# Kernel tuning notes

Hardware: AMD Instinct MI355X
Metric: run time of the kernel (lower is better)

## Reference

```python
import jax, jax.numpy as jnp
import numpy as np

D_MODEL = 1024
NUM_HEADS = 16
HEAD_DIM = D_MODEL // NUM_HEADS


def setup_inputs() -> dict:
    key = jax.random.key(0)
    ks = jax.random.split(key, 9)
    B, S = 2, 2048
    s = 1.0 / np.sqrt(D_MODEL)
    inp = {
        "x": jax.random.normal(ks[0], (B, S, D_MODEL), dtype=jnp.float32),
        "Wq": jax.random.normal(ks[1], (D_MODEL, D_MODEL), dtype=jnp.float32) * s,
        "bq": jnp.zeros((D_MODEL,), dtype=jnp.float32),
        "Wk": jax.random.normal(ks[2], (D_MODEL, D_MODEL), dtype=jnp.float32) * s,
        "bk": jnp.zeros((D_MODEL,), dtype=jnp.float32),
        "Wv": jax.random.normal(ks[3], (D_MODEL, D_MODEL), dtype=jnp.float32) * s,
        "bv": jnp.zeros((D_MODEL,), dtype=jnp.float32),
        "Wo": jax.random.normal(ks[4], (D_MODEL, D_MODEL), dtype=jnp.float32) * s,
        "bo": jnpp if False else jnp.zeros((D_MODEL,), dtype=jnp.float32),
    }
    return inp


def reference(x, Wq, bq, Wk, bk, Wv, bv, Wo, bo):
    B, S, D = x.shape
    H, hd = NUM_HEADS, HEAD_DIM
    # QKV projections (Linear: x @ W^T + b), split into heads -> [B,H,S,hd]
    q = (x @ Wq.T + bq).reshape(B, S, H, hd).transpose(0, 2, 1, 3)
    k = (x @ Wk.T + bk).reshape(B, S, H, hd).transpose(0, 2, 1, 3)
    v = (x @ Wv.T + bv).reshape(B, S, H, hd).transpose(0, 2, 1, 3)
    # scores [B,H,S,S]
    scores = jnp.einsum('bhqd,bhkd->bhqk', q, k) / jnp.sqrt(jnp.float32(hd))
    p = jax.nn.softmax(scores, axis=-1)
    out = jnp.einsum('bhqk,bhkd->bhqd', p, v)  # [B,H,S,hd]
    out = out.transpose(0, 2, 1, 3).reshape(B, S, D)
    return out @ Wo.T + bo
```

## Files before the change

kernel.cpp:

```cpp
#include <hip/hip_runtime.h>
#include <hip/hip_bf16.h>
#include <math.h>

typedef __bf16 bf16;
typedef unsigned short u16;
typedef __bf16 bf16x8 __attribute__((ext_vector_type(8)));
typedef __bf16 bf16x4 __attribute__((ext_vector_type(4)));
typedef short  s16x4  __attribute__((ext_vector_type(4)));
typedef float  f32x4  __attribute__((ext_vector_type(4)));

#define D_MODEL 1024
#define NHEAD   16
#define HD      64
#define BATCH   2
#define SEQ     2048
#define MTOT    (BATCH*SEQ)

#define EXPSCALE 0.18033688011116016f

__device__ __forceinline__ void async16(const void* g, void* l) {
    __builtin_amdgcn_global_load_lds(
        (__attribute__((address_space(1))) unsigned int*)g,
        (__attribute__((address_space(3))) unsigned int*)l,
        16, 0, 0);
}

__device__ __forceinline__ f32x4 mfma16(s16x4 a, s16x4 b, f32x4 c) {
    return __builtin_amdgcn_mfma_f32_16x16x16bf16_1k(a, b, c, 0, 0, 0);
}

__global__ __launch_bounds__(256) void cast_kernel(
    const float* __restrict__ x,
    const float* __restrict__ wq, const float* __restrict__ wk,
    const float* __restrict__ wv, const float* __restrict__ wo,
    bf16* __restrict__ xb, bf16* __restrict__ wqb, bf16* __restrict__ wkb,
    bf16* __restrict__ wvb, bf16* __restrict__ wob)
{
    const int z = blockIdx.y;
    const float* src;
    bf16* dst;
    int n;
    if (z == 0)      { src = x;  dst = xb;  n = MTOT * D_MODEL; }
    else if (z == 1) { src = wq; dst = wqb; n = D_MODEL * D_MODEL; }
    else if (z == 2) { src = wk; dst = wkb; n = D_MODEL * D_MODEL; }
    else if (z == 3) { src = wv; dst = wvb; n = D_MODEL * D_MODEL; }
    else             { src = wo; dst = wob; n = D_MODEL * D_MODEL; }

    int i = (blockIdx.x * 256 + threadIdx.x) * 8;
    if (i >= n) return;
    float4 a = *(const float4*)(src + i);
    float4 b = *(const float4*)(src + i + 4);
    bf16x8 o;
    o[0] = (bf16)a.x; o[1] = (bf16)a.y; o[2] = (bf16)a.z; o[3] = (bf16)a.w;
    o[4] = (bf16)b.x; o[5] = (bf16)b.y; o[6] = (bf16)b.z; o[7] = (bf16)b.w;
    *(bf16x8*)(dst + i) = o;
}

__device__ __forceinline__ void gemm_core(const bf16* __restrict__ A,
                                          const bf16* __restrict__ W,
                                          int m0, int n0,
                                          f32x4 acc[4][4],
                                          u16* lA, u16* lB)
{
    const int tid  = threadIdx.x;
    const int lane = tid & 63;
    const int wave = tid >> 6;
    const int wr   = wave >> 1;
    const int wc   = wave & 1;
    const int fr   = lane & 15;
    const int quad = lane >> 4;

    #pragma unroll
    for (int mi = 0; mi < 4; ++mi)
        #pragma unroll
        for (int ni = 0; ni < 4; ++ni)
            #pragma unroll
            for (int e = 0; e < 4; ++e)
                acc[mi][ni][e] = 0.0f;

    const int row = tid >> 3;
    const int ca  = ((tid & 7) ^ (row & 7)) * 8;
    const bf16* gA[4];
    const bf16* gB[4];
    u16 *sA[4], *sB[4];
    #pragma unroll
    for (int c = 0; c < 4; ++c) {
        int slot = tid + c * 256;
        int r    = row + c * 32;
        gA[c] = A + (size_t)(m0 + r) * 1024 + ca;
        gB[c] = W + (size_t)(n0 + r) * 1024 + ca;
        sA[c] = lA + (size_t)slot * 8;
        sB[c] = lB + (size_t)slot * 8;
    }

    for (int kt = 0; kt < 1024 / 64; ++kt) {
        __syncthreads();
        #pragma unroll
        for (int c = 0; c < 4; ++c) {
            async16(gA[c] + kt * 64, sA[c]);
            async16(gB[c] + kt * 64, sB[c]);
        }
        __syncthreads();

        #pragma unroll
        for (int ks = 0; ks < 2; ++ks) {
            const int sa = ((ks * 4 + quad) ^ (fr & 7)) * 8;
            bf16x8 af[4], bfm[4];
            #pragma unroll
            for (int mi = 0; mi < 4; ++mi)
                af[mi] = *(const bf16x8*)(lA + (wr * 64 + mi * 16 + fr) * 64 + sa);
            #pragma unroll
            for (int ni = 0; ni < 4; ++ni)
                bfm[ni] = *(const bf16x8*)(lB + (wc * 64 + ni * 16 + fr) * 64 + sa);

            #pragma unroll
            for (int mi = 0; mi < 4; ++mi)
                #pragma unroll
                for (int ni = 0; ni < 4; ++ni)
                    acc[mi][ni] = __builtin_amdgcn_mfma_f32_16x16x32_bf16(
                        af[mi], bfm[ni], acc[mi][ni], 0, 0, 0);
        }
    }
}

__global__ __launch_bounds__(256) void qkv_kernel(
    const bf16* __restrict__ x,
    const bf16* __restrict__ Wq, const bf16* __restrict__ Wk, const bf16* __restrict__ Wv,
    const float* __restrict__ bq, const float* __restrict__ bk, const float* __restrict__ bv,
    bf16* __restrict__ Q, bf16* __restrict__ K, bf16* __restrict__ Vt)
{
    __shared__ __align__(16) u16 lA[128 * 64];
    __shared__ __align__(16) u16 lB[128 * 64];

    const int z = blockIdx.z;
    int m0, n0;
    const bf16 *mA, *mB;
    const float* bias;
    if (z == 2) {
        mA = Wv; mB = x; bias = bv;
        m0 = blockIdx.y * 128;
        n0 = blockIdx.x * 128;
    } else {
        mA = x;  mB = (z == 0) ? Wq : Wk; bias = (z == 0) ? bq : bk;
        m0 = blockIdx.x * 128;
        n0 = blockIdx.y * 128;
    }

    f32x4 acc[4][4];
    gemm_core(mA, mB, m0, n0, acc, lA, lB);

    const int lane = threadIdx.x & 63;
    const int wave = threadIdx.x >> 6;
    const int wr = wave >> 1, wc = wave & 1;
    const int col = lane & 15, quad = lane >> 4;

    if (z == 2) {
        #pragma unroll
        for (int mi = 0; mi < 4; ++mi) {
            #pragma unroll
            for (int ni = 0; ni < 4; ++ni) {
                #pragma unroll
                for (int r = 0; r < 4; ++r) {
                    int f = m0 + wr * 64 + mi * 16 + quad * 4 + r;
                    int t = n0 + wc * 64 + ni * 16 + col;
                    float v = acc[mi][ni][r] + bias[f];
                    int b = t >> 11, s = t & 2047;
                    int h = f >> 6,  d = f & 63;
                    Vt[((size_t)(b * NHEAD + h) * HD + d) * SEQ + s] = (bf16)v;
                }
            }
        }
    } else {
        const float qs = (z == 0) ? EXPSCALE : 1.0f;
        bf16* o = (z == 0) ? Q : K;
        #pragma unroll
        for (int mi = 0; mi < 4; ++mi) {
            #pragma unroll
            for (int ni = 0; ni < 4; ++ni) {
                #pragma unroll
                for (int r = 0; r < 4; ++r) {
                    int m = m0 + wr * 64 + mi * 16 + quad * 4 + r;
                    int n = n0 + wc * 64 + ni * 16 + col;
                    float v = (acc[mi][ni][r] + bias[n]) * qs;
                    int b = m >> 11, s = m & 2047;
                    int h = n >> 6,  d = n & 63;
                    o[((size_t)(b * NHEAD + h) * SEQ + s) * HD + d] = (bf16)v;
                }
            }
        }
    }
}

__global__ __launch_bounds__(256, 2) void attn_kernel(
    const bf16* __restrict__ Q, const bf16* __restrict__ K,
    const bf16* __restrict__ Vt, bf16* __restrict__ O)
{
    __shared__ __align__(16) u16 lK[2][64 * 64];
    __shared__ __align__(16) u16 lV[2][64 * 64];

    const int tid  = threadIdx.x;
    const int lane = tid & 63;
    const int wave = tid >> 6;
    const int col  = lane & 15;
    const int quad = lane >> 4;
    const int bh   = blockIdx.x;
    const int q0   = blockIdx.y * 128;

    const bf16* Qh = Q  + (size_t)bh * SEQ * HD;
    const bf16* Kh = K  + (size_t)bh * SEQ * HD;
    const bf16* Vh = Vt + (size_t)bh * HD * SEQ;

    bf16x8 qf[2][2];
    #pragma unroll
    for (int qb = 0; qb < 2; ++qb)
        #pragma unroll
        for (int ks = 0; ks < 2; ++ks)
            qf[qb][ks] = *(const bf16x8*)(
                Qh + (size_t)(q0 + wave * 32 + qb * 16 + col) * HD + ks * 32 + quad * 8);

    f32x4 acc_o[2][4];
    #pragma unroll
    for (int qb = 0; qb < 2; ++qb)
        #pragma unroll
        for (int nd = 0; nd < 4; ++nd)
            #pragma unroll
            for (int e = 0; e < 4; ++e) acc_o[qb][nd][e] = 0.0f;
    float rs[2] = {0.0f, 0.0f};
    const f32x4 zero4 = {0.0f, 0.0f, 0.0f, 0.0f};

    const int r0 = tid >> 3;
    const int r1 = r0 + 32;
    const int g0 = (((tid & 7) ^ (r0 & 7))) * 8;
    const int g1 = (((tid & 7) ^ (r1 & 7))) * 8;
    const bf16* gK0 = Kh + (size_t)r0 * HD + g0;
    const bf16* gK1 = Kh + (size_t)r1 * HD + g1;
    const bf16* gV0 = Vh + (size_t)r0 * SEQ + g0;
    const bf16* gV1 = Vh + (size_t)r1 * SEQ + g1;
    const int so0 = tid * 8;
    const int so1 = (tid + 256) * 8;

    async16(gK0, lK[0] + so0);
    async16(gK1, lK[0] + so1);
    async16(gV0, lV[0] + so0);
    async16(gV1, lV[0] + so1);

    int cur = 0;
    for (int jt = 0; jt < SEQ / 64; ++jt) {
        __syncthreads();

        if (jt + 1 < SEQ / 64) {
            const int nx = cur ^ 1;
            async16(gK0 + (size_t)(jt + 1) * 64 * HD, lK[nx] + so0);
            async16(gK1 + (size_t)(jt + 1) * 64 * HD, lK[nx] + so1);
            async16(gV0 + (jt + 1) * 64, lV[nx] + so0);
            async16(gV1 + (jt + 1) * 64, lV[nx] + so1);
        }

        const u16* K_ = lK[cur];
        const u16* V_ = lV[cur];

        f32x4 sc[2][4];
        #pragma unroll
        for (int nj = 0; nj < 4; ++nj) {
            bf16x8 kf0 = *(const bf16x8*)(
                K_ + (nj * 16 + col) * 64 + ((0 + quad) ^ (col & 7)) * 8);
            sc[0][nj] = __builtin_amdgcn_mfma_f32_16x16x32_bf16(kf0, qf[0][0], zero4, 0, 0, 0);
            sc[1][nj] = __builtin_amdgcn_mfma_f32_16x16x32_bf16(kf0, qf[1][0], zero4, 0, 0, 0);
        }
        #pragma unroll
        for (int nj = 0; nj < 4; ++nj) {
            bf16x8 kf1 = *(const bf16x8*)(
                K_ + (nj * 16 + col) * 64 + ((4 + quad) ^ (col & 7)) * 8);
            sc[0][nj] = __builtin_amdgcn_mfma_f32_16x16x32_bf16(kf1, qf[0][1], sc[0][nj], 0, 0, 0);
            sc[1][nj] = __builtin_amdgcn_mfma_f32_16x16x32_bf16(kf1, qf[1][1], sc[1][nj], 0, 0, 0);
        }

        s16x4 pb[2][4];
        #pragma unroll
        for (int qb = 0; qb < 2; ++qb) {
            #pragma unroll
            for (int nj = 0; nj < 4; ++nj) {
                float p0 = __builtin_amdgcn_exp2f(sc[qb][nj][0]);
                float p1 = __builtin_amdgcn_exp2f(sc[qb][nj][1]);
                float p2 = __builtin_amdgcn_exp2f(sc[qb][nj][2]);
                float p3 = __builtin_amdgcn_exp2f(sc[qb][nj][3]);
                rs[qb] += (p0 + p1) + (p2 + p3);
                bf16x4 t;
                t[0] = (bf16)p0; t[1] = (bf16)p1; t[2] = (bf16)p2; t[3] = (bf16)p3;
                pb[qb][nj] = __builtin_bit_cast(s16x4, t);
            }
        }

        #pragma unroll
        for (int nj = 0; nj < 4; ++nj) {
            #pragma unroll
            for (int nd = 0; nd < 4; ++nd) {
                int row = nd * 16 + col;
                int jb  = (2 * nj + (quad >> 1)) ^ (row & 7);
                s16x4 vb = *(const s16x4*)(V_ + row * 64 + jb * 8 + (quad & 1) * 4);
                acc_o[0][nd] = mfma16(pb[0][nj], vb, acc_o[0][nd]);
                acc_o[1][nd] = mfma16(pb[1][nj], vb, acc_o[1][nd]);
            }
        }

        cur ^= 1;
    }

    const int b = bh >> 4, h = bh & 15;
    #pragma unroll
    for (int qb = 0; qb < 2; ++qb) {
        float v = rs[qb];
        v += __shfl_xor(v, 16);
        v += __shfl_xor(v, 32);
        float inv = 1.0f / v;
        float invr[4];
        #pragma unroll
        for (int r = 0; r < 4; ++r)
            invr[r] = __shfl(inv, quad * 4 + r);
        #pragma unroll
        for (int nd = 0; nd < 4; ++nd) {
            #pragma unroll
            for (int r = 0; r < 4; ++r) {
                int srow = q0 + wave * 32 + qb * 16 + quad * 4 + r;
                int d    = nd * 16 + col;
                float o  = acc_o[qb][nd][r] * invr[r];
                O[((size_t)(b * SEQ + srow)) * D_MODEL + h * HD + d] = (bf16)o;
            }
        }
    }
}

__global__ __launch_bounds__(256) void oproj_kernel(
    const bf16* __restrict__ A, const bf16* __restrict__ Wo,
    const float* __restrict__ bo, float* __restrict__ out)
{
    __shared__ __align__(16) u16 lA[128 * 64];
    __shared__ __align__(16) u16 lB[64 * 64];

    const int m0 = blockIdx.x * 128;
    const int n0 = blockIdx.y * 64;

    const int tid  = threadIdx.x;
    const int lane = tid & 63;
    const int wave = tid >> 6;
    const int wr   = wave >> 1;
    const int wc   = wave & 1;
    const int fr   = lane & 15;
    const int quad = lane >> 4;

    f32x4 acc[4][2];
    #pragma unroll
    for (int mi = 0; mi < 4; ++mi)
        #pragma unroll
        for (int ni = 0; ni < 2; ++ni)
            #pragma unroll
            for (int e = 0; e < 4; ++e)
                acc[mi][ni][e] = 0.0f;

    const int row = tid >> 3;
    const int ca  = ((tid & 7) ^ (row & 7)) * 8;
    const bf16* gA[4];
    u16* sA[4];
    #pragma unroll
    for (int c = 0; c < 4; ++c) {
        int slot = tid + c * 256;
        gA[c] = A + (size_t)(m0 + row + c * 32) * 1024 + ca;
        sA[c] = lA + (size_t)slot * 8;
    }
    const bf16* gB[2];
    u16* sB[2];
    #pragma unroll
    for (int c = 0; c < 2; ++c) {
        int slot = tid + c * 256;
        gB[c] = Wo + (size_t)(n0 + row + c * 32) * 1024 + ca;
        sB[c] = lB + (size_t)slot * 8;
    }

    for (int kt = 0; kt < 1024 / 64; ++kt) {
        __syncthreads();
        #pragma unroll
        for (int c = 0; c < 4; ++c) async16(gA[c] + kt * 64, sA[c]);
        #pragma unroll
        for (int c = 0; c < 2; ++c) async16(gB[c] + kt * 64, sB[c]);
        __syncthreads();

        #pragma unroll
        for (int ks = 0; ks < 2; ++ks) {
            const int sa = ((ks * 4 + quad) ^ (fr & 7)) * 8;
            bf16x8 af[4], bfm[2];
            #pragma unroll
            for (int mi = 0; mi < 4; ++mi)
                af[mi] = *(const bf16x8*)(lA + (wr * 64 + mi * 16 + fr) * 64 + sa);
            #pragma unroll
            for (int ni = 0; ni < 2; ++ni)
                bfm[ni] = *(const bf16x8*)(lB + (wc * 32 + ni * 16 + fr) * 64 + sa);

            #pragma unroll
            for (int mi = 0; mi < 4; ++mi)
                #pragma unroll
                for (int ni = 0; ni < 2; ++ni)
                    acc[mi][ni] = __builtin_amdgcn_mfma_f32_16x16x32_bf16(
                        af[mi], bfm[ni], acc[mi][ni], 0, 0, 0);
        }
    }

    const int col = fr;
    #pragma unroll
    for (int mi = 0; mi < 4; ++mi) {
        #pragma unroll
        for (int ni = 0; ni < 2; ++ni) {
            #pragma unroll
            for (int r = 0; r < 4; ++r) {
                int m = m0 + wr * 64 + mi * 16 + quad * 4 + r;
                int n = n0 + wc * 32 + ni * 16 + col;
                out[(size_t)m * D_MODEL + n] = acc[mi][ni][r] + bo[n];
            }
        }
    }
}

extern "C" void kernel_launch(void* const* d_in, const int* in_sizes, int n_in,
                              void* d_out, int out_size, void* d_ws, size_t ws_size,
                              hipStream_t stream)
{
    const float* x  = (const float*)d_in[0];
    const float* Wq = (const float*)d_in[1];
    const float* bq = (const float*)d_in[2];
    const float* Wk = (const float*)d_in[3];
    const float* bk = (const float*)d_in[4];
    const float* Wv = (const float*)d_in[5];
    const float* bv = (const float*)d_in[6];
    const float* Wo = (const float*)d_in[7];
    const float* bo = (const float*)d_in[8];
    float* out = (float*)d_out;

    char* ws = (char*)d_ws;
    const size_t XSZ = (size_t)MTOT * D_MODEL * sizeof(bf16);
    const size_t WSZ = (size_t)D_MODEL * D_MODEL * sizeof(bf16);
    bf16* wqb = (bf16*)(ws);
    bf16* wkb = (bf16*)(ws + WSZ);
    bf16* wvb = (bf16*)(ws + 2 * WSZ);
    bf16* wob = (bf16*)(ws + 3 * WSZ);
    bf16* xb  = (bf16*)(ws + 4 * WSZ);
    bf16* Qb  = (bf16*)(ws + 4 * WSZ + XSZ);
    bf16* Kb  = (bf16*)(ws + 4 * WSZ + 2 * XSZ);
    bf16* Vt  = (bf16*)(ws + 4 * WSZ + 3 * XSZ);
    bf16* At  = (bf16*)(ws + 4 * WSZ + 4 * XSZ);

    cast_kernel<<<dim3((MTOT * D_MODEL) / (256 * 8), 5), 256, 0, stream>>>(
        x, Wq, Wk, Wv, Wo, xb, wqb, wkb, wvb, wob);

    qkv_kernel<<<dim3(32, 8, 3), 256, 0, stream>>>(
        xb, wqb, wkb, wvb, bq, bk, bv, Qb, Kb, Vt);

    attn_kernel<<<dim3(BATCH * NHEAD, SEQ / 128), 256, 0, stream>>>(Qb, Kb, Vt, At);

    oproj_kernel<<<dim3(MTOT / 128, D_MODEL / 64), 256, 0, stream>>>(At, wob, bo, out);
}
```

Before: 195.2 us.

## Software-pipeline attention: overlap PV of previous tile with QK of current tile

Restructures the attention inner loop so the P·V MFMAs for the previous key tile run alongside the QK^T MFMAs for the current tile, with the softmax exp work issued afterwards at lower wave priority. K rows are loaded into LDS in a permuted order so that P fragments map directly onto 16x16x32 MFMA operands, replacing the 16x16x16 PV MFMAs and halving their count. V loads are delayed by one iteration and a drain step after the loop handles the last tile. The P fragments must stay live across iterations, which raises register pressure, and the s_setprio hints may or may not help the scheduler.

```diff
diff --git a/kernel.cpp b/kernel.cpp
--- a/kernel.cpp
+++ b/kernel.cpp
@@ -5,8 +5,6 @@
 typedef __bf16 bf16;
 typedef unsigned short u16;
 typedef __bf16 bf16x8 __attribute__((ext_vector_type(8)));
-typedef __bf16 bf16x4 __attribute__((ext_vector_type(4)));
-typedef short  s16x4  __attribute__((ext_vector_type(4)));
 typedef float  f32x4  __attribute__((ext_vector_type(4)));
 
 #define D_MODEL 1024
@@ -23,10 +21,6 @@
         (__attribute__((address_space(1))) unsigned int*)g,
         (__attribute__((address_space(3))) unsigned int*)l,
         16, 0, 0);
-}
-
-__device__ __forceinline__ f32x4 mfma16(s16x4 a, s16x4 b, f32x4 c) {
-    return __builtin_amdgcn_mfma_f32_16x16x16bf16_1k(a, b, c, 0, 0, 0);
 }
 
 __global__ __launch_bounds__(256) void cast_kernel(
@@ -205,6 +199,7 @@
     const int quad = lane >> 4;
     const int bh   = blockIdx.x;
     const int q0   = blockIdx.y * 128;
+    const int NT   = SEQ / 64;
 
     const bf16* Qh = Q  + (size_t)bh * SEQ * HD;
     const bf16* Kh = K  + (size_t)bh * SEQ * HD;
@@ -229,81 +224,107 @@
     const f32x4 zero4 = {0.0f, 0.0f, 0.0f, 0.0f};
 
     const int r0 = tid >> 3;
-    const int r1 = r0 + 32;
-    const int g0 = (((tid & 7) ^ (r0 & 7))) * 8;
-    const int g1 = (((tid & 7) ^ (r1 & 7))) * 8;
-    const bf16* gK0 = Kh + (size_t)r0 * HD + g0;
-    const bf16* gK1 = Kh + (size_t)r1 * HD + g1;
+    const int jp = ((((r0 >> 2) & 3) << 3) | (((r0 >> 4) & 1) << 2) | (r0 & 3));
+    const int g0 = ((tid & 7) ^ (r0 & 7)) * 8;
+    const bf16* gK0 = Kh + (size_t)jp * HD + g0;
+    const bf16* gK1 = Kh + (size_t)(jp + 32) * HD + g0;
     const bf16* gV0 = Vh + (size_t)r0 * SEQ + g0;
-    const bf16* gV1 = Vh + (size_t)r1 * SEQ + g1;
+    const bf16* gV1 = Vh + (size_t)(r0 + 32) * SEQ + g0;
     const int so0 = tid * 8;
     const int so1 = (tid + 256) * 8;
 
     async16(gK0, lK[0] + so0);
     async16(gK1, lK[0] + so1);
-    async16(gV0, lV[0] + so0);
-    async16(gV1, lV[0] + so1);
-
-    int cur = 0;
-    for (int jt = 0; jt < SEQ / 64; ++jt) {
+
+    bf16x8 pa0[2], pa1[2];
+
+    for (int jt = 0; jt < NT; ++jt) {
         __syncthreads();
 
-        if (jt + 1 < SEQ / 64) {
-            const int nx = cur ^ 1;
-            async16(gK0 + (size_t)(jt + 1) * 64 * HD, lK[nx] + so0);
-            async16(gK1 + (size_t)(jt + 1) * 64 * HD, lK[nx] + so1);
-            async16(gV0 + (jt + 1) * 64, lV[nx] + so0);
-            async16(gV1 + (jt + 1) * 64, lV[nx] + so1);
-        }
-
-        const u16* K_ = lK[cur];
-        const u16* V_ = lV[cur];
-
-        f32x4 sc[2][4];
+        if (jt + 1 < NT) {
+            async16(gK0 + (size_t)(jt + 1) * 64 * HD, lK[(jt + 1) & 1] + so0);
+            async16(gK1 + (size_t)(jt + 1) * 64 * HD, lK[(jt + 1) & 1] + so1);
+        }
+        async16(gV0 + jt * 64, lV[jt & 1] + so0);
+        async16(gV1 + jt * 64, lV[jt & 1] + so1);
+
+        const u16* K_ = lK[jt & 1];
+
+        __builtin_amdgcn_s_setprio(1);
+
+        f32x4 sc0[4], sc1[4];
         #pragma unroll
         for (int nj = 0; nj < 4; ++nj) {
             bf16x8 kf0 = *(const bf16x8*)(
                 K_ + (nj * 16 + col) * 64 + ((0 + quad) ^ (col & 7)) * 8);
-            sc[0][nj] = __builtin_amdgcn_mfma_f32_16x16x32_bf16(kf0, qf[0][0], zero4, 0, 0, 0);
-            sc[1][nj] = __builtin_amdgcn_mfma_f32_16x16x32_bf16(kf0, qf[1][0], zero4, 0, 0, 0);
+            sc0[nj] = __builtin_amdgcn_mfma_f32_16x16x32_bf16(kf0, qf[0][0], zero4, 0, 0, 0);
+            sc1[nj] = __builtin_amdgcn_mfma_f32_16x16x32_bf16(kf0, qf[1][0], zero4, 0, 0, 0);
         }
         #pragma unroll
         for (int nj = 0; nj < 4; ++nj) {
             bf16x8 kf1 = *(const bf16x8*)(
                 K_ + (nj * 16 + col) * 64 + ((4 + quad) ^ (col & 7)) * 8);
-            sc[0][nj] = __builtin_amdgcn_mfma_f32_16x16x32_bf16(kf1, qf[0][1], sc[0][nj], 0, 0, 0);
-            sc[1][nj] = __builtin_amdgcn_mfma_f32_16x16x32_bf16(kf1, qf[1][1], sc[1][nj], 0, 0, 0);
-        }
-
-        s16x4 pb[2][4];
-        #pragma unroll
-        for (int qb = 0; qb < 2; ++qb) {
-            #pragma unroll
-            for (int nj = 0; nj < 4; ++nj) {
-                float p0 = __builtin_amdgcn_exp2f(sc[qb][nj][0]);
-                float p1 = __builtin_amdgcn_exp2f(sc[qb][nj][1]);
-                float p2 = __builtin_amdgcn_exp2f(sc[qb][nj][2]);
-                float p3 = __builtin_amdgcn_exp2f(sc[qb][nj][3]);
-                rs[qb] += (p0 + p1) + (p2 + p3);
-                bf16x4 t;
-                t[0] = (bf16)p0; t[1] = (bf16)p1; t[2] = (bf16)p2; t[3] = (bf16)p3;
-                pb[qb][nj] = __builtin_bit_cast(s16x4, t);
-            }
-        }
-
-        #pragma unroll
-        for (int nj = 0; nj < 4; ++nj) {
+            sc0[nj] = __builtin_amdgcn_mfma_f32_16x16x32_bf16(kf1, qf[0][1], sc0[nj], 0, 0, 0);
+            sc1[nj] = __builtin_amdgcn_mfma_f32_16x16x32_bf16(kf1, qf[1][1], sc1[nj], 0, 0, 0);
+        }
+
+        if (jt > 0) {
+            const u16* V_ = lV[(jt - 1) & 1];
+            #pragma unroll
+            for (int c = 0; c < 2; ++c) {
+                #pragma unroll
+                for (int nd = 0; nd < 4; ++nd) {
+                    int row = nd * 16 + col;
+                    int b   = (c * 4 + quad) ^ (row & 7);
+                    bf16x8 vb = *(const bf16x8*)(V_ + row * 64 + b * 8);
+                    acc_o[0][nd] = __builtin_amdgcn_mfma_f32_16x16x32_bf16(
+                        pa0[c], vb, acc_o[0][nd], 0, 0, 0);
+                    acc_o[1][nd] = __builtin_amdgcn_mfma_f32_16x16x32_bf16(
+                        pa1[c], vb, acc_o[1][nd], 0, 0, 0);
+                }
+            }
+        }
+
+        __builtin_amdgcn_s_setprio(0);
+
+        #pragma unroll
+        for (int c = 0; c < 2; ++c) {
+            bf16x8 t0, t1;
+            #pragma unroll
+            for (int e = 0; e < 4; ++e) {
+                float a = __builtin_amdgcn_exp2f(sc0[2 * c][e]);
+                float b = __builtin_amdgcn_exp2f(sc0[2 * c + 1][e]);
+                rs[0] += a + b;
+                t0[e]     = (bf16)a;
+                t0[4 + e] = (bf16)b;
+                float a1 = __builtin_amdgcn_exp2f(sc1[2 * c][e]);
+                float b1 = __builtin_amdgcn_exp2f(sc1[2 * c + 1][e]);
+                rs[1] += a1 + b1;
+                t1[e]     = (bf16)a1;
+                t1[4 + e] = (bf16)b1;
+            }
+            pa0[c] = t0;
+            pa1[c] = t1;
+        }
+    }
+
+    __syncthreads();
+
+    {
+        const u16* V_ = lV[(NT - 1) & 1];
+        #pragma unroll
+        for (int c = 0; c < 2; ++c) {
             #pragma unroll
             for (int nd = 0; nd < 4; ++nd) {
                 int row = nd * 16 + col;
-                int jb  = (2 * nj + (quad >> 1)) ^ (row & 7);
-                s16x4 vb = *(const s16x4*)(V_ + row * 64 + jb * 8 + (quad & 1) * 4);
-                acc_o[0][nd] = mfma16(pb[0][nj], vb, acc_o[0][nd]);
-                acc_o[1][nd] = mfma16(pb[1][nj], vb, acc_o[1][nd]);
-            }
-        }
-
-        cur ^= 1;
+                int b   = (c * 4 + quad) ^ (row & 7);
+                bf16x8 vb = *(const bf16x8*)(V_ + row * 64 + b * 8);
+                acc_o[0][nd] = __builtin_amdgcn_mfma_f32_16x16x32_bf16(
+                    pa0[c], vb, acc_o[0][nd], 0, 0, 0);
+                acc_o[1][nd] = __builtin_amdgcn_mfma_f32_16x16x32_bf16(
+                    pa1[c], vb, acc_o[1][nd], 0, 0, 0);
+            }
+        }
     }
 
     const int b = bh >> 4, h = bh & 15;
```

New measurement: 188.1 us. 1.04x faster.
